# Kernel tuning notes

Measured on AMD Instinct MI355X. Metric: run time of the kernel, lower is better.

The kernel has to match this reference:

```python
import jax, jax.numpy as jnp
import numpy as np

B, S, D = 32, 1024, 256
K, H, L = 64, 4, 4
KH, DV = K // H, D // H  # pooling key size per head, pooling value size
EPS = 1e-5
SCALE = 1.0 / np.sqrt(K).astype(np.float32)  # both encoder and pooling use sqrt(1/key_size)


def _ln(x, gamma=None, beta=None):
    m = jnp.mean(x, axis=-1, keepdims=True)
    v = jnp.mean(jnp.square(x - m), axis=-1, keepdims=True)
    y = (x - m) * jax.lax.rsqrt(v + EPS)
    if gamma is not None:
        y = y * gamma + beta
    return y


def setup_inputs() -> dict:
    key = jax.random.key(0)
    ks = iter(jax.random.split(key, 32))

    def w(shape, fan_in):
        return jax.random.normal(next(ks), shape, jnp.float32) / np.sqrt(fan_in).astype(np.float32)

    inp = {
        "input": jax.random.normal(next(ks), (B, S, D), jnp.float32),
        "lin0_W": w((D, D), D), "lin0_b": jnp.zeros((D,), jnp.float32),
        # stacked params for the 4 AttentionEncoder layers
        "enc_Wk": w((L, D, K), D), "enc_bk": jnp.zeros((L, K), jnp.float32),
        "enc_Wq": w((L, D, K), D), "enc_bq": jnp.zeros((L, K), jnp.float32),
        "enc_Wv": w((L, D, D), D), "enc_bv": jnp.zeros((L, D), jnp.float32),
        "enc_Wb": w((L, D, 1), D), "enc_bb": jnp.zeros((L, 1), jnp.float32),
        "enc_Wff": w((L, D, D), D), "enc_bff": jnp.zeros((L, D), jnp.float32),
        "enc_g1": jnp.ones((L, D), jnp.float32), "enc_beta1": jnp.zeros((L, D), jnp.float32),
        # multi-head pooling head
        "pool_Wk": w((D, KH), D), "pool_bk": jnp.zeros((KH,), jnp.float32),
        "pool_Wv": w((D, DV), D), "pool_bv": jnp.zeros((DV,), jnp.float32),
        "queries": jax.random.normal(next(ks), (H, KH), jnp.float32),
        "lin1_W": w((D, 2), D), "lin1_b": jnp.zeros((2,), jnp.float32),
    }
    return inp


def reference(input, lin0_W, lin0_b, enc_Wk, enc_bk, enc_Wq, enc_bq, enc_Wv, enc_bv,
              enc_Wb, enc_bb, enc_Wff, enc_bff, enc_g1, enc_beta1,
              pool_Wk, pool_bk, pool_Wv, pool_bv, queries, lin1_W, lin1_b):
    # NOTE: original code computes act0(lin0(input)) and then discards it (dead code);
    # it is omitted here since it does not affect the output.
    x = input
    for i in range(L):
        k = (x @ enc_Wk[i] + enc_bk[i]) * SCALE          # [B,S,K]
        q = x @ enc_Wq[i] + enc_bq[i]                     # [B,S,K]
        v = x @ enc_Wv[i] + enc_bv[i]                     # [B,S,D]
        bias = x @ enc_Wb[i] + enc_bb[i]                  # [B,S,1], broadcast over columns
        scores = jax.nn.sigmoid(jnp.einsum('bik,bjk->bij', k, q) + bias)  # [B,S,S]
        attn = jnp.einsum('bij,bjd->bid', scores, v)      # [B,S,D]
        res = _ln(x + attn, enc_g1[i], enc_beta1[i])
        ff = jax.nn.relu(res @ enc_Wff[i] + enc_bff[i])
        x = _ln(res + ff)                                 # norm2: no affine
    # multi-head pooling with learned queries
    pk = (x @ pool_Wk + pool_bk) * SCALE                  # [B,S,KH]
    pv = x @ pool_Wv + pool_bv                            # [B,S,DV]
    sc = jnp.einsum('bsk,hk->bsh', pk, queries)           # [B,S,H]
    sc = jax.nn.softmax(sc, axis=1)                       # softmax over sequence
    pooled = jnp.einsum('bsh,bsd->bhd', sc, pv).reshape(x.shape[0], -1)  # [B, H*DV]=[B,D]
    return pooled @ lin1_W + lin1_b                       # [B,2]
```

## Files before the change

kernel.cpp:

```cpp
#include <hip/hip_runtime.h>
#include <hip/hip_bf16.h>
#include <math.h>

#define BB 32
#define SS 1024
#define DD 256
#define MM (BB*SS)
#define LEPS 1e-5f

typedef __bf16 bf16x8 __attribute__((ext_vector_type(8)));
typedef __bf16 bf16x4 __attribute__((ext_vector_type(4)));
typedef float f32x4 __attribute__((ext_vector_type(4)));

__global__ __launch_bounds__(256) void cast_wt(const float* __restrict__ W,
                                               __bf16* __restrict__ WT,
                                               int N, float scale, int dstride, int noff) {
    int n = blockIdx.x, l = blockIdx.z, k = threadIdx.x;
    WT[(size_t)dstride * l + (size_t)(n + noff) * 256 + k] =
        (__bf16)(W[(size_t)256 * N * l + (size_t)k * N + n] * scale);
}

__global__ __launch_bounds__(128) void bias_combine(const float* __restrict__ bk,
                                                    const float* __restrict__ bq,
                                                    float* __restrict__ dst) {
    int l = blockIdx.x, j = threadIdx.x;
    dst[l * 128 + j] = (j < 64) ? bk[l * 64 + j] * 0.125f : bq[l * 64 + (j - 64)];
}

__global__ __launch_bounds__(256) void cast_x(const float* __restrict__ x, __bf16* __restrict__ xb) {
    size_t i = ((size_t)blockIdx.x * 256 + threadIdx.x) * 8;
    float4 a = *(const float4*)(x + i);
    float4 b = *(const float4*)(x + i + 4);
    __bf16 o[8] __attribute__((aligned(16)));
    o[0] = (__bf16)a.x; o[1] = (__bf16)a.y; o[2] = (__bf16)a.z; o[3] = (__bf16)a.w;
    o[4] = (__bf16)b.x; o[5] = (__bf16)b.y; o[6] = (__bf16)b.z; o[7] = (__bf16)b.w;
    *(bf16x8*)(xb + i) = *(bf16x8*)o;
}

template <int BN, int MODE>
__global__ __launch_bounds__(256) void gemm_mfma(const __bf16* __restrict__ A,
                                                 const __bf16* __restrict__ WT,
                                                 const float* __restrict__ bias,
                                                 float bscale, int relu,
                                                 void* __restrict__ Cv, void* __restrict__ Cv2,
                                                 int N) {
    constexpr int MR = (BN == 128) ? 4 : 2;
    constexpr int NC = (BN == 128) ? 4 : BN / 16;
    const int t = threadIdx.x;
    const int w = t >> 6, lane = t & 63;
    const int m0 = blockIdx.x * 128;
    const int n0 = blockIdx.y * BN;
    const size_t wt_z = (MODE == 3) ? (size_t)blockIdx.z * SS * 256 : 0;
    const size_t c_z  = (MODE == 3) ? (size_t)blockIdx.z * 256 * (size_t)N : 0;
    const int wr = (BN == 128) ? (w >> 1) * 64 : w * 32;
    const int wc = (BN == 128) ? (w & 1) * 64 : 0;
    __shared__ __align__(16) __bf16 Al[128][64];
    __shared__ __align__(16) __bf16 Wl[BN][64];
    f32x4 acc[MR][NC] = {};

    for (int k0 = 0; k0 < 256; k0 += 64) {
        __syncthreads();
        {
            int r = t >> 1, half = t & 1;
            const __bf16* src = A + (size_t)(m0 + r) * 256 + k0 + half * 32;
            bf16x8 v0 = *(const bf16x8*)(src);
            bf16x8 v1 = *(const bf16x8*)(src + 8);
            bf16x8 v2 = *(const bf16x8*)(src + 16);
            bf16x8 v3 = *(const bf16x8*)(src + 24);
            int cb = half * 4;
            *(bf16x8*)&Al[r][((cb + 0) ^ (r & 7)) * 8] = v0;
            *(bf16x8*)&Al[r][((cb + 1) ^ (r & 7)) * 8] = v1;
            *(bf16x8*)&Al[r][((cb + 2) ^ (r & 7)) * 8] = v2;
            *(bf16x8*)&Al[r][((cb + 3) ^ (r & 7)) * 8] = v3;
        }
        if (BN == 128) {
            int r = t >> 1, half = t & 1;
            const __bf16* src = WT + wt_z + (size_t)(n0 + r) * 256 + k0 + half * 32;
            bf16x8 v0 = *(const bf16x8*)(src);
            bf16x8 v1 = *(const bf16x8*)(src + 8);
            bf16x8 v2 = *(const bf16x8*)(src + 16);
            bf16x8 v3 = *(const bf16x8*)(src + 24);
            int cb = half * 4;
            *(bf16x8*)&Wl[r][((cb + 0) ^ (r & 7)) * 8] = v0;
            *(bf16x8*)&Wl[r][((cb + 1) ^ (r & 7)) * 8] = v1;
            *(bf16x8*)&Wl[r][((cb + 2) ^ (r & 7)) * 8] = v2;
            *(bf16x8*)&Wl[r][((cb + 3) ^ (r & 7)) * 8] = v3;
        } else if (BN == 64) {
            int n = t >> 2, q = t & 3;
            const __bf16* src = WT + (size_t)(n0 + n) * 256 + k0 + q * 16;
            bf16x8 v0 = *(const bf16x8*)src;
            bf16x8 v1 = *(const bf16x8*)(src + 8);
            *(bf16x8*)&Wl[n][((q * 2 + 0) ^ (n & 7)) * 8] = v0;
            *(bf16x8*)&Wl[n][((q * 2 + 1) ^ (n & 7)) * 8] = v1;
        } else {
            if (t < 128) {
                int n = t >> 3, c = t & 7;
                bf16x8 v = *(const bf16x8*)(WT + (size_t)(n0 + n) * 256 + k0 + c * 8);
                *(bf16x8*)&Wl[n][(c ^ (n & 7)) * 8] = v;
            }
        }
        __syncthreads();
#pragma unroll
        for (int ks = 0; ks < 2; ks++) {
            int c = ks * 4 + (lane >> 4);
            bf16x8 af[MR];
#pragma unroll
            for (int mf = 0; mf < MR; mf++) {
                int i = wr + mf * 16 + (lane & 15);
                af[mf] = *(const bf16x8*)&Al[i][(c ^ (i & 7)) * 8];
            }
#pragma unroll
            for (int nf = 0; nf < NC; nf++) {
                int n = wc + nf * 16 + (lane & 15);
                bf16x8 bfr = *(const bf16x8*)&Wl[n][(c ^ (n & 7)) * 8];
#pragma unroll
                for (int mf = 0; mf < MR; mf++)
                    acc[mf][nf] = __builtin_amdgcn_mfma_f32_16x16x32_bf16(af[mf], bfr, acc[mf][nf], 0, 0, 0);
            }
        }
    }
#pragma unroll
    for (int mf = 0; mf < MR; mf++) {
#pragma unroll
        for (int nf = 0; nf < NC; nf++) {
            int col = n0 + wc + nf * 16 + (lane & 15);
            float bcol = (MODE == 3) ? 0.f : bias[col] * bscale;
#pragma unroll
            for (int r = 0; r < 4; r++) {
                int row = m0 + wr + mf * 16 + (lane >> 4) * 4 + r;
                float v = acc[mf][nf][r] + ((MODE == 3) ? bias[row] : bcol);
                if (relu) v = fmaxf(v, 0.f);
                if (MODE == 2) {
                    if (col < 64) ((__bf16*)Cv)[(size_t)row * 64 + col] = (__bf16)v;
                    else ((__bf16*)Cv2)[(size_t)row * 64 + (col - 64)] = (__bf16)v;
                } else if (MODE == 1 || MODE == 3) {
                    ((__bf16*)Cv)[c_z + (size_t)row * N + col] = (__bf16)v;
                } else {
                    ((float*)Cv)[(size_t)row * N + col] = v;
                }
            }
        }
    }
}

__global__ __launch_bounds__(256) void bias_gemv(const __bf16* __restrict__ X,
                                                 const float* __restrict__ Wb,
                                                 const float* __restrict__ bb,
                                                 float* __restrict__ out) {
    int wave = threadIdx.x >> 6, lane = threadIdx.x & 63;
    size_t row = (size_t)blockIdx.x * 4 + wave;
    bf16x4 xv = *(const bf16x4*)(X + row * 256 + lane * 4);
    float4 wv = *(const float4*)(Wb + lane * 4);
    float p = (float)xv[0] * wv.x + (float)xv[1] * wv.y + (float)xv[2] * wv.z + (float)xv[3] * wv.w;
    for (int off = 32; off; off >>= 1) p += __shfl_down(p, off, 64);
    if (lane == 0) out[row] = p + bb[0];
}

__global__ __launch_bounds__(512, 4) void attn_mfma(const __bf16* __restrict__ kb,
                                                    const __bf16* __restrict__ qb,
                                                    const __bf16* __restrict__ vT,
                                                    const float* __restrict__ biasb,
                                                    const __bf16* __restrict__ xinb,
                                                    const float* __restrict__ gamma,
                                                    const float* __restrict__ beta,
                                                    __bf16* __restrict__ outb) {
    int h = blockIdx.x;
    int blow = h & 7, rest = h >> 3;
    int ib = rest & 15;
    int b = blow + (rest >> 4) * 8;
    const int i0 = ib * 64;
    const int t = threadIdx.x;
    const int w = t >> 6, lane = t & 63;
    const int iq = w >> 1;
    const int dhalf = w & 1;

    __shared__ __align__(16) __bf16 Kl[64][64];
    __shared__ __align__(16) __bf16 Ql[64][64];
    __shared__ __align__(16) __bf16 Vl[256][64];
    __shared__ __align__(16) __bf16 Sl[64][64];
    __shared__ float bsh[64];
    __shared__ float rowred[2][64][2];

    const int qj = t >> 3, qc = t & 7;
    const __bf16* qsrc_base = qb + ((size_t)(b * SS + qj)) * 64 + qc * 8;
    const int vd = t >> 1, vjh = t & 1;
    const __bf16* vsrc_base = vT + ((size_t)b * 256 + vd) * SS + vjh * 32;

    {
        int i = t >> 3, c = t & 7;
        bf16x8 v = *(const bf16x8*)(kb + ((size_t)(b * SS + i0 + i)) * 64 + c * 8);
        *(bf16x8*)&Kl[i][(c ^ (i & 7)) * 8] = v;
        if (t < 64) bsh[t] = biasb[b * SS + i0 + t];
    }
    {
        bf16x8 qv = *(const bf16x8*)(qsrc_base);
        *(bf16x8*)&Ql[qj][(qc ^ (qj & 7)) * 8] = qv;
#pragma unroll
        for (int u = 0; u < 4; u++) {
            bf16x8 v = *(const bf16x8*)(vsrc_base + u * 8);
            *(bf16x8*)&Vl[vd][((vjh * 4 + u) ^ (vd & 7)) * 8] = v;
        }
    }
    __syncthreads();

    f32x4 acc[8] = {};

    for (int j0 = 0; j0 < SS; j0 += 64) {
        const bool has_next = (j0 + 64) < SS;
        bf16x8 qn;
        bf16x8 vn0, vn1, vn2, vn3;
        if (has_next) {
            qn = *(const bf16x8*)(qsrc_base + (size_t)(j0 + 64) * 64);
            const __bf16* vs = vsrc_base + j0 + 64;
            vn0 = *(const bf16x8*)(vs);
            vn1 = *(const bf16x8*)(vs + 8);
            vn2 = *(const bf16x8*)(vs + 16);
            vn3 = *(const bf16x8*)(vs + 24);
        }
#pragma unroll
        for (int jj = 0; jj < 2; jj++) {
            int jq = (w & 1) * 2 + jj;
            f32x4 sacc = {0.f, 0.f, 0.f, 0.f};
            __builtin_amdgcn_s_setprio(1);
#pragma unroll
            for (int ks = 0; ks < 2; ks++) {
                int i = iq * 16 + (lane & 15);
                int ck = ks * 4 + (lane >> 4);
                bf16x8 a = *(const bf16x8*)&Kl[i][(ck ^ (i & 7)) * 8];
                int j = jq * 16 + (lane & 15);
                bf16x8 bq = *(const bf16x8*)&Ql[j][(ck ^ (j & 7)) * 8];
                sacc = __builtin_amdgcn_mfma_f32_16x16x32_bf16(a, bq, sacc, 0, 0, 0);
            }
            __builtin_amdgcn_s_setprio(0);
            int jcol = jq * 16 + (lane & 15);
#pragma unroll
            for (int r = 0; r < 4; r++) {
                int irow = iq * 16 + (lane >> 4) * 4 + r;
                float x = sacc[r] + bsh[irow];
                float sg = 1.f / (1.f + __expf(-x));
                Sl[irow][(((jcol >> 3) ^ (irow & 7)) * 8) + (jcol & 7)] = (__bf16)sg;
            }
        }
        __syncthreads();
        bf16x8 am[2];
#pragma unroll
        for (int m = 0; m < 2; m++) {
            int i = iq * 16 + (lane & 15);
            int cj = m * 4 + (lane >> 4);
            am[m] = *(const bf16x8*)&Sl[i][(cj ^ (i & 7)) * 8];
        }
        __builtin_amdgcn_s_setprio(1);
#pragma unroll
        for (int dq = 0; dq < 8; dq++) {
            int d = dhalf * 128 + dq * 16 + (lane & 15);
#pragma unroll
            for (int m = 0; m < 2; m++) {
                int cj = m * 4 + (lane >> 4);
                bf16x8 bv = *(const bf16x8*)&Vl[d][(cj ^ (d & 7)) * 8];
                acc[dq] = __builtin_amdgcn_mfma_f32_16x16x32_bf16(am[m], bv, acc[dq], 0, 0, 0);
            }
        }
        __builtin_amdgcn_s_setprio(0);
        __syncthreads();
        if (has_next) {
            *(bf16x8*)&Ql[qj][(qc ^ (qj & 7)) * 8] = qn;
            *(bf16x8*)&Vl[vd][((vjh * 4 + 0) ^ (vd & 7)) * 8] = vn0;
            *(bf16x8*)&Vl[vd][((vjh * 4 + 1) ^ (vd & 7)) * 8] = vn1;
            *(bf16x8*)&Vl[vd][((vjh * 4 + 2) ^ (vd & 7)) * 8] = vn2;
            *(bf16x8*)&Vl[vd][((vjh * 4 + 3) ^ (vd & 7)) * 8] = vn3;
            __syncthreads();
        }
    }

#pragma unroll
    for (int r = 0; r < 4; r++) {
        int il = iq * 16 + (lane >> 4) * 4 + r;
        size_t rowoff = ((size_t)(b * SS + i0 + il)) * 256 + dhalf * 128 + (lane & 15);
#pragma unroll
        for (int dq = 0; dq < 8; dq++)
            acc[dq][r] += (float)xinb[rowoff + dq * 16];
    }
    float sr[4], qr[4];
#pragma unroll
    for (int r = 0; r < 4; r++) {
        float s = 0.f, q = 0.f;
#pragma unroll
        for (int dq = 0; dq < 8; dq++) {
            float v = acc[dq][r];
            s += v; q += v * v;
        }
#pragma unroll
        for (int mask = 8; mask; mask >>= 1) {
            s += __shfl_xor(s, mask, 64);
            q += __shfl_xor(q, mask, 64);
        }
        sr[r] = s; qr[r] = q;
    }
    if ((lane & 15) == 0) {
#pragma unroll
        for (int r = 0; r < 4; r++) {
            int il = iq * 16 + (lane >> 4) * 4 + r;
            rowred[dhalf][il][0] = sr[r];
            rowred[dhalf][il][1] = qr[r];
        }
    }
    __syncthreads();
    float gv[8], bv2[8];
#pragma unroll
    for (int dq = 0; dq < 8; dq++) {
        int d = dhalf * 128 + dq * 16 + (lane & 15);
        gv[dq] = gamma[d];
        bv2[dq] = beta[d];
    }
#pragma unroll
    for (int r = 0; r < 4; r++) {
        int il = iq * 16 + (lane >> 4) * 4 + r;
        float st = rowred[0][il][0] + rowred[1][il][0];
        float qt = rowred[0][il][1] + rowred[1][il][1];
        float mean = st * (1.f / 256.f);
        float var = qt * (1.f / 256.f) - mean * mean;
        float inv = 1.f / sqrtf(var + LEPS);
        size_t rowoff = ((size_t)(b * SS + i0 + il)) * 256 + dhalf * 128 + (lane & 15);
#pragma unroll
        for (int dq = 0; dq < 8; dq++) {
            float o = (acc[dq][r] - mean) * inv * gv[dq] + bv2[dq];
            outb[rowoff + dq * 16] = (__bf16)o;
        }
    }
}

__global__ __launch_bounds__(512) void gemm_ff_ln2(const __bf16* __restrict__ A,
                                                   const __bf16* __restrict__ WT,
                                                   const float* __restrict__ bias,
                                                   const __bf16* __restrict__ resid,
                                                   __bf16* __restrict__ outb) {
    const int t = threadIdx.x;
    const int w = t >> 6, lane = t & 63;
    const int m0 = blockIdx.x * 128;
    const int wr = (w >> 2) * 64, wc = (w & 3) * 64;
    __shared__ __align__(16) __bf16 Al[128][64];
    __shared__ __align__(16) __bf16 Wl[256][64];
    __shared__ float rowred[4][128][2];
    f32x4 acc[4][4] = {};

    for (int k0 = 0; k0 < 256; k0 += 64) {
        __syncthreads();
        {
            int r = t >> 2, c0 = (t & 3) * 2;
            const __bf16* src = A + (size_t)(m0 + r) * 256 + k0 + c0 * 8;
            bf16x8 v0 = *(const bf16x8*)src;
            bf16x8 v1 = *(const bf16x8*)(src + 8);
            *(bf16x8*)&Al[r][((c0 + 0) ^ (r & 7)) * 8] = v0;
            *(bf16x8*)&Al[r][((c0 + 1) ^ (r & 7)) * 8] = v1;
        }
        {
            int n = t >> 1, c0 = (t & 1) * 4;
            const __bf16* src = WT + (size_t)n * 256 + k0 + c0 * 8;
#pragma unroll
            for (int u = 0; u < 4; u++) {
                bf16x8 v = *(const bf16x8*)(src + u * 8);
                *(bf16x8*)&Wl[n][((c0 + u) ^ (n & 7)) * 8] = v;
            }
        }
        __syncthreads();
#pragma unroll
        for (int ks = 0; ks < 2; ks++) {
            int c = ks * 4 + (lane >> 4);
            bf16x8 af[4];
#pragma unroll
            for (int mf = 0; mf < 4; mf++) {
                int i = wr + mf * 16 + (lane & 15);
                af[mf] = *(const bf16x8*)&Al[i][(c ^ (i & 7)) * 8];
            }
#pragma unroll
            for (int nf = 0; nf < 4; nf++) {
                int n = wc + nf * 16 + (lane & 15);
                bf16x8 bfr = *(const bf16x8*)&Wl[n][(c ^ (n & 7)) * 8];
#pragma unroll
                for (int mf = 0; mf < 4; mf++)
                    acc[mf][nf] = __builtin_amdgcn_mfma_f32_16x16x32_bf16(af[mf], bfr, acc[mf][nf], 0, 0, 0);
            }
        }
    }
    float colb[4];
#pragma unroll
    for (int nf = 0; nf < 4; nf++) colb[nf] = bias[wc + nf * 16 + (lane & 15)];
#pragma unroll
    for (int mf = 0; mf < 4; mf++) {
#pragma unroll
        for (int r = 0; r < 4; r++) {
            int rl = wr + mf * 16 + (lane >> 4) * 4 + r;
            const __bf16* rrow = resid + (size_t)(m0 + rl) * 256 + wc + (lane & 15);
            float s = 0.f, q = 0.f;
#pragma unroll
            for (int nf = 0; nf < 4; nf++) {
                float v = fmaxf(acc[mf][nf][r] + colb[nf], 0.f) + (float)rrow[nf * 16];
                acc[mf][nf][r] = v;
                s += v; q += v * v;
            }
#pragma unroll
            for (int msk = 1; msk <= 8; msk <<= 1) {
                s += __shfl_xor(s, msk, 64);
                q += __shfl_xor(q, msk, 64);
            }
            if ((lane & 15) == 0) {
                rowred[w & 3][rl][0] = s;
                rowred[w & 3][rl][1] = q;
            }
        }
    }
    __syncthreads();
#pragma unroll
    for (int mf = 0; mf < 4; mf++) {
#pragma unroll
        for (int r = 0; r < 4; r++) {
            int rl = wr + mf * 16 + (lane >> 4) * 4 + r;
            float s = rowred[0][rl][0] + rowred[1][rl][0] + rowred[2][rl][0] + rowred[3][rl][0];
            float q = rowred[0][rl][1] + rowred[1][rl][1] + rowred[2][rl][1] + rowred[3][rl][1];
            float mean = s * (1.f / 256.f);
            float var = q * (1.f / 256.f) - mean * mean;
            float inv = 1.f / sqrtf(var + LEPS);
            size_t base = (size_t)(m0 + rl) * 256 + wc + (lane & 15);
#pragma unroll
            for (int nf = 0; nf < 4; nf++) {
                float o = (acc[mf][nf][r] - mean) * inv;
                outb[base + nf * 16] = (__bf16)o;
            }
        }
    }
}

__global__ __launch_bounds__(1024) void pool_kernel(const float* __restrict__ pk,
                                                    const float* __restrict__ pv,
                                                    const float* __restrict__ queries,
                                                    const float* __restrict__ W1,
                                                    const float* __restrict__ b1,
                                                    float* __restrict__ out) {
    const int b = blockIdx.x;
    const int t = threadIdx.x;
    __shared__ float sc[4][1024];
    __shared__ float qv[4][16];
    __shared__ float redsum[4];
    __shared__ float psum[4][256];
    __shared__ float r0[256], r1[256];
    if (t < 64) qv[t >> 4][t & 15] = queries[t];
    __syncthreads();
    {
        int s = t;
        const float* p = pk + ((size_t)b * SS + s) * 16;
        float4 a0 = *(const float4*)p;
        float4 a1 = *(const float4*)(p + 4);
        float4 a2 = *(const float4*)(p + 8);
        float4 a3 = *(const float4*)(p + 12);
#pragma unroll
        for (int hh = 0; hh < 4; hh++) {
            float d = a0.x * qv[hh][0] + a0.y * qv[hh][1] + a0.z * qv[hh][2] + a0.w * qv[hh][3]
                    + a1.x * qv[hh][4] + a1.y * qv[hh][5] + a1.z * qv[hh][6] + a1.w * qv[hh][7]
                    + a2.x * qv[hh][8] + a2.y * qv[hh][9] + a2.z * qv[hh][10] + a2.w * qv[hh][11]
                    + a3.x * qv[hh][12] + a3.y * qv[hh][13] + a3.z * qv[hh][14] + a3.w * qv[hh][15];
            sc[hh][s] = d;
        }
    }
    __syncthreads();
    if (t < 256) {
        int hh = t >> 6, lane = t & 63;
        float m = -1e30f;
        for (int s = lane; s < 1024; s += 64) m = fmaxf(m, sc[hh][s]);
        for (int off = 32; off; off >>= 1) m = fmaxf(m, __shfl_down(m, off, 64));
        m = __shfl(m, 0, 64);
        float sum = 0.f;
        for (int s = lane; s < 1024; s += 64) {
            float e = expf(sc[hh][s] - m);
            sc[hh][s] = e;
            sum += e;
        }
        for (int off = 32; off; off >>= 1) sum += __shfl_down(sum, off, 64);
        if (lane == 0) redsum[hh] = sum;
    }
    __syncthreads();
    {
        int chunk = t >> 8, pair = t & 255;
        int hh = pair >> 6, d = pair & 63;
        float a = 0.f;
        int s0 = chunk * 256;
        for (int s = s0; s < s0 + 256; s++)
            a += sc[hh][s] * pv[((size_t)b * SS + s) * 64 + d];
        psum[chunk][pair] = a;
    }
    __syncthreads();
    if (t < 256) {
        float a = (psum[0][t] + psum[1][t] + psum[2][t] + psum[3][t]) / redsum[t >> 6];
        r0[t] = a * W1[t * 2 + 0];
        r1[t] = a * W1[t * 2 + 1];
    }
    __syncthreads();
    for (int off = 128; off > 0; off >>= 1) {
        if (t < off) { r0[t] += r0[t + off]; r1[t] += r1[t + off]; }
        __syncthreads();
    }
    if (t == 0) {
        out[b * 2 + 0] = r0[0] + b1[0];
        out[b * 2 + 1] = r1[0] + b1[1];
    }
}

extern "C" void kernel_launch(void* const* d_in, const int* in_sizes, int n_in,
                              void* d_out, int out_size, void* d_ws, size_t ws_size,
                              hipStream_t stream) {
    const float* input = (const float*)d_in[0];
    const float* eWk = (const float*)d_in[3];
    const float* ebk = (const float*)d_in[4];
    const float* eWq = (const float*)d_in[5];
    const float* ebq = (const float*)d_in[6];
    const float* eWv = (const float*)d_in[7];
    const float* ebv = (const float*)d_in[8];
    const float* eWb = (const float*)d_in[9];
    const float* ebb = (const float*)d_in[10];
    const float* eWff = (const float*)d_in[11];
    const float* ebff = (const float*)d_in[12];
    const float* eg1 = (const float*)d_in[13];
    const float* ebe1 = (const float*)d_in[14];
    const float* pWk = (const float*)d_in[15];
    const float* pbk = (const float*)d_in[16];
    const float* pWv = (const float*)d_in[17];
    const float* pbv = (const float*)d_in[18];
    const float* qrs = (const float*)d_in[19];
    const float* W1 = (const float*)d_in[20];
    const float* b1 = (const float*)d_in[21];
    float* out = (float*)d_out;

    float* ws = (float*)d_ws;
    float* xbuf = ws;
    __bf16* xbf = (__bf16*)(xbuf + (size_t)MM * DD);
    float* tmp2 = (float*)(xbf + (size_t)MM * DD);
    float* r3 = tmp2 + (size_t)MM * DD;
    __bf16* tmp2bf = (__bf16*)r3;
    __bf16* vTb = tmp2bf + (size_t)MM * DD;
    float* r4 = r3 + (size_t)MM * DD;
    __bf16* kbf = (__bf16*)r4;
    __bf16* qbf = kbf + (size_t)MM * 64;
    float* bbuf = r4 + (size_t)MM * (DD / 2);
    __bf16* wbf = (__bf16*)(bbuf + MM);

    __bf16* WkqT = wbf;
    __bf16* WvT = WkqT + 4 * 128 * 256;
    __bf16* WffT = WvT + 4 * 256 * 256;
    __bf16* pWkT = WffT + 4 * 256 * 256;
    __bf16* pWvT = pWkT + 16 * 256;
    float* biasc = (float*)(pWvT + 64 * 256);

    float* pkbuf = tmp2;
    float* pvbuf = tmp2 + (size_t)MM * 16;

    const float SC = 0.125f;

    cast_wt<<<dim3(64, 1, 4), 256, 0, stream>>>(eWk, WkqT, 64, SC, 128 * 256, 0);
    cast_wt<<<dim3(64, 1, 4), 256, 0, stream>>>(eWq, WkqT, 64, 1.f, 128 * 256, 64);
    cast_wt<<<dim3(256, 1, 4), 256, 0, stream>>>(eWv, WvT, 256, 1.f, 256 * 256, 0);
    cast_wt<<<dim3(256, 1, 4), 256, 0, stream>>>(eWff, WffT, 256, 1.f, 256 * 256, 0);
    cast_wt<<<dim3(16, 1, 1), 256, 0, stream>>>(pWk, pWkT, 16, SC, 16 * 256, 0);
    cast_wt<<<dim3(64, 1, 1), 256, 0, stream>>>(pWv, pWvT, 64, 1.f, 64 * 256, 0);
    bias_combine<<<4, 128, 0, stream>>>(ebk, ebq, biasc);
    cast_x<<<MM * DD / (256 * 8), 256, 0, stream>>>(input, xbf);

    for (int l = 0; l < 4; l++) {
        gemm_mfma<128, 2><<<dim3(MM / 128, 1), 256, 0, stream>>>(
            xbf, WkqT + (size_t)l * 128 * 256, biasc + l * 128, 1.f, 0, kbf, qbf, 64);
        gemm_mfma<128, 3><<<dim3(2, SS / 128, BB), 256, 0, stream>>>(
            WvT + (size_t)l * 256 * 256, xbf, ebv + l * DD, 1.f, 0, vTb, nullptr, SS);
        bias_gemv<<<MM / 4, 256, 0, stream>>>(xbf, eWb + (size_t)l * DD, ebb + l, bbuf);
        attn_mfma<<<dim3(512, 1), 512, 0, stream>>>(kbf, qbf, vTb, bbuf, xbf,
                                                    eg1 + l * DD, ebe1 + l * DD, tmp2bf);
        gemm_ff_ln2<<<dim3(MM / 128, 1), 512, 0, stream>>>(
            tmp2bf, WffT + (size_t)l * 256 * 256, ebff + l * DD, tmp2bf, xbf);
    }
    gemm_mfma<16, 0><<<dim3(MM / 128, 1), 256, 0, stream>>>(xbf, pWkT, pbk, SC, 0, pkbuf, nullptr, 16);
    gemm_mfma<64, 0><<<dim3(MM / 128, 1), 256, 0, stream>>>(xbf, pWvT, pbv, 1.f, 0, pvbuf, nullptr, 64);
    pool_kernel<<<BB, 1024, 0, stream>>>(pkbuf, pvbuf, qrs, W1, b1, out);
}
```

Before: 488.0 us.

## Re-split attention PV tiles across warps and parallelize pooling into three kernels

In the attention kernel, each of the 8 warps now owns a 32-column slice of D across all 64 query rows, instead of a 16-row by 128-column tile. Each V fragment loaded from LDS is therefore reused across 4 row groups, and the LayerNorm reduction is rebuilt to combine partial sums from all 8 warps. The pooling head, which was a single 32-block kernel, is split into a softmax kernel, a chunked weighted-sum kernel, and a final reduction kernel. The split gives the GPU more blocks to run at once, at the cost of extra launches and intermediate buffers in global memory.

Measured after the change: 477.8 us. 1.02x faster.

```diff
diff --git a/kernel.cpp b/kernel.cpp
--- a/kernel.cpp
+++ b/kernel.cpp
@@ -172,14 +172,13 @@
     const int t = threadIdx.x;
     const int w = t >> 6, lane = t & 63;
     const int iq = w >> 1;
-    const int dhalf = w & 1;
 
     __shared__ __align__(16) __bf16 Kl[64][64];
     __shared__ __align__(16) __bf16 Ql[64][64];
     __shared__ __align__(16) __bf16 Vl[256][64];
     __shared__ __align__(16) __bf16 Sl[64][64];
     __shared__ float bsh[64];
-    __shared__ float rowred[2][64][2];
+    __shared__ float rowred[8][64][2];
 
     const int qj = t >> 3, qc = t & 7;
     const __bf16* qsrc_base = qb + ((size_t)(b * SS + qj)) * 64 + qc * 8;
@@ -203,7 +202,7 @@
     }
     __syncthreads();
 
-    f32x4 acc[8] = {};
+    f32x4 acc[4][2] = {};
 
     for (int j0 = 0; j0 < SS; j0 += 64) {
         const bool has_next = (j0 + 64) < SS;
@@ -242,22 +241,23 @@
             }
         }
         __syncthreads();
-        bf16x8 am[2];
+        __builtin_amdgcn_s_setprio(1);
 #pragma unroll
         for (int m = 0; m < 2; m++) {
-            int i = iq * 16 + (lane & 15);
             int cj = m * 4 + (lane >> 4);
-            am[m] = *(const bf16x8*)&Sl[i][(cj ^ (i & 7)) * 8];
-        }
-        __builtin_amdgcn_s_setprio(1);
-#pragma unroll
-        for (int dq = 0; dq < 8; dq++) {
-            int d = dhalf * 128 + dq * 16 + (lane & 15);
-#pragma unroll
-            for (int m = 0; m < 2; m++) {
-                int cj = m * 4 + (lane >> 4);
+            bf16x8 am[4];
+#pragma unroll
+            for (int ig = 0; ig < 4; ig++) {
+                int i = ig * 16 + (lane & 15);
+                am[ig] = *(const bf16x8*)&Sl[i][(cj ^ (i & 7)) * 8];
+            }
+#pragma unroll
+            for (int dt = 0; dt < 2; dt++) {
+                int d = w * 32 + dt * 16 + (lane & 15);
                 bf16x8 bv = *(const bf16x8*)&Vl[d][(cj ^ (d & 7)) * 8];
-                acc[dq] = __builtin_amdgcn_mfma_f32_16x16x32_bf16(am[m], bv, acc[dq], 0, 0, 0);
+#pragma unroll
+                for (int ig = 0; ig < 4; ig++)
+                    acc[ig][dt] = __builtin_amdgcn_mfma_f32_16x16x32_bf16(am[ig], bv, acc[ig][dt], 0, 0, 0);
             }
         }
         __builtin_amdgcn_s_setprio(0);
@@ -273,58 +273,45 @@
     }
 
 #pragma unroll
-    for (int r = 0; r < 4; r++) {
-        int il = iq * 16 + (lane >> 4) * 4 + r;
-        size_t rowoff = ((size_t)(b * SS + i0 + il)) * 256 + dhalf * 128 + (lane & 15);
-#pragma unroll
-        for (int dq = 0; dq < 8; dq++)
-            acc[dq][r] += (float)xinb[rowoff + dq * 16];
-    }
-    float sr[4], qr[4];
-#pragma unroll
-    for (int r = 0; r < 4; r++) {
-        float s = 0.f, q = 0.f;
-#pragma unroll
-        for (int dq = 0; dq < 8; dq++) {
-            float v = acc[dq][r];
-            s += v; q += v * v;
-        }
-#pragma unroll
-        for (int mask = 8; mask; mask >>= 1) {
-            s += __shfl_xor(s, mask, 64);
-            q += __shfl_xor(q, mask, 64);
-        }
-        sr[r] = s; qr[r] = q;
-    }
-    if ((lane & 15) == 0) {
+    for (int ig = 0; ig < 4; ig++) {
 #pragma unroll
         for (int r = 0; r < 4; r++) {
-            int il = iq * 16 + (lane >> 4) * 4 + r;
-            rowred[dhalf][il][0] = sr[r];
-            rowred[dhalf][il][1] = qr[r];
-        }
-    }
-    __syncthreads();
-    float gv[8], bv2[8];
-#pragma unroll
-    for (int dq = 0; dq < 8; dq++) {
-        int d = dhalf * 128 + dq * 16 + (lane & 15);
-        gv[dq] = gamma[d];
-        bv2[dq] = beta[d];
-    }
-#pragma unroll
-    for (int r = 0; r < 4; r++) {
-        int il = iq * 16 + (lane >> 4) * 4 + r;
-        float st = rowred[0][il][0] + rowred[1][il][0];
-        float qt = rowred[0][il][1] + rowred[1][il][1];
-        float mean = st * (1.f / 256.f);
-        float var = qt * (1.f / 256.f) - mean * mean;
-        float inv = 1.f / sqrtf(var + LEPS);
-        size_t rowoff = ((size_t)(b * SS + i0 + il)) * 256 + dhalf * 128 + (lane & 15);
-#pragma unroll
-        for (int dq = 0; dq < 8; dq++) {
-            float o = (acc[dq][r] - mean) * inv * gv[dq] + bv2[dq];
-            outb[rowoff + dq * 16] = (__bf16)o;
+            int il = ig * 16 + (lane >> 4) * 4 + r;
+            size_t rowoff = ((size_t)(b * SS + i0 + il)) * 256 + w * 32 + (lane & 15);
+            float v0 = acc[ig][0][r] + (float)xinb[rowoff];
+            float v1 = acc[ig][1][r] + (float)xinb[rowoff + 16];
+            acc[ig][0][r] = v0; acc[ig][1][r] = v1;
+            float s = v0 + v1, q = v0 * v0 + v1 * v1;
+#pragma unroll
+            for (int mask = 8; mask; mask >>= 1) {
+                s += __shfl_xor(s, mask, 64);
+                q += __shfl_xor(q, mask, 64);
+            }
+            if ((lane & 15) == 0) {
+                rowred[w][il][0] = s;
+                rowred[w][il][1] = q;
+            }
+        }
+    }
+    __syncthreads();
+    float gv0 = gamma[w * 32 + (lane & 15)];
+    float gv1 = gamma[w * 32 + 16 + (lane & 15)];
+    float be0 = beta[w * 32 + (lane & 15)];
+    float be1 = beta[w * 32 + 16 + (lane & 15)];
+#pragma unroll
+    for (int ig = 0; ig < 4; ig++) {
+#pragma unroll
+        for (int r = 0; r < 4; r++) {
+            int il = ig * 16 + (lane >> 4) * 4 + r;
+            float s = 0.f, q = 0.f;
+#pragma unroll
+            for (int ww = 0; ww < 8; ww++) { s += rowred[ww][il][0]; q += rowred[ww][il][1]; }
+            float mean = s * (1.f / 256.f);
+            float var = q * (1.f / 256.f) - mean * mean;
+            float inv = 1.f / sqrtf(var + LEPS);
+            size_t rowoff = ((size_t)(b * SS + i0 + il)) * 256 + w * 32 + (lane & 15);
+            outb[rowoff]      = (__bf16)((acc[ig][0][r] - mean) * inv * gv0 + be0);
+            outb[rowoff + 16] = (__bf16)((acc[ig][1][r] - mean) * inv * gv1 + be1);
         }
     }
 }
@@ -430,69 +417,72 @@
     }
 }
 
-__global__ __launch_bounds__(1024) void pool_kernel(const float* __restrict__ pk,
-                                                    const float* __restrict__ pv,
+__global__ __launch_bounds__(256) void pool_softmax(const float* __restrict__ pk,
                                                     const float* __restrict__ queries,
-                                                    const float* __restrict__ W1,
-                                                    const float* __restrict__ b1,
-                                                    float* __restrict__ out) {
-    const int b = blockIdx.x;
+                                                    float* __restrict__ wout) {
+    const int b = blockIdx.x, h = blockIdx.y;
     const int t = threadIdx.x;
-    __shared__ float sc[4][1024];
-    __shared__ float qv[4][16];
-    __shared__ float redsum[4];
-    __shared__ float psum[4][256];
-    __shared__ float r0[256], r1[256];
-    if (t < 64) qv[t >> 4][t & 15] = queries[t];
-    __syncthreads();
-    {
-        int s = t;
+    const int wv = t >> 6, lane = t & 63;
+    __shared__ float qv[16];
+    __shared__ float redm[4], reds[4];
+    if (t < 16) qv[t] = queries[h * 16 + t];
+    __syncthreads();
+    float sc[4];
+#pragma unroll
+    for (int c = 0; c < 4; c++) {
+        int s = c * 256 + t;
         const float* p = pk + ((size_t)b * SS + s) * 16;
         float4 a0 = *(const float4*)p;
         float4 a1 = *(const float4*)(p + 4);
         float4 a2 = *(const float4*)(p + 8);
         float4 a3 = *(const float4*)(p + 12);
-#pragma unroll
-        for (int hh = 0; hh < 4; hh++) {
-            float d = a0.x * qv[hh][0] + a0.y * qv[hh][1] + a0.z * qv[hh][2] + a0.w * qv[hh][3]
-                    + a1.x * qv[hh][4] + a1.y * qv[hh][5] + a1.z * qv[hh][6] + a1.w * qv[hh][7]
-                    + a2.x * qv[hh][8] + a2.y * qv[hh][9] + a2.z * qv[hh][10] + a2.w * qv[hh][11]
-                    + a3.x * qv[hh][12] + a3.y * qv[hh][13] + a3.z * qv[hh][14] + a3.w * qv[hh][15];
-            sc[hh][s] = d;
-        }
-    }
-    __syncthreads();
-    if (t < 256) {
-        int hh = t >> 6, lane = t & 63;
-        float m = -1e30f;
-        for (int s = lane; s < 1024; s += 64) m = fmaxf(m, sc[hh][s]);
-        for (int off = 32; off; off >>= 1) m = fmaxf(m, __shfl_down(m, off, 64));
-        m = __shfl(m, 0, 64);
-        float sum = 0.f;
-        for (int s = lane; s < 1024; s += 64) {
-            float e = expf(sc[hh][s] - m);
-            sc[hh][s] = e;
-            sum += e;
-        }
-        for (int off = 32; off; off >>= 1) sum += __shfl_down(sum, off, 64);
-        if (lane == 0) redsum[hh] = sum;
-    }
-    __syncthreads();
-    {
-        int chunk = t >> 8, pair = t & 255;
-        int hh = pair >> 6, d = pair & 63;
-        float a = 0.f;
-        int s0 = chunk * 256;
-        for (int s = s0; s < s0 + 256; s++)
-            a += sc[hh][s] * pv[((size_t)b * SS + s) * 64 + d];
-        psum[chunk][pair] = a;
-    }
-    __syncthreads();
-    if (t < 256) {
-        float a = (psum[0][t] + psum[1][t] + psum[2][t] + psum[3][t]) / redsum[t >> 6];
-        r0[t] = a * W1[t * 2 + 0];
-        r1[t] = a * W1[t * 2 + 1];
-    }
+        sc[c] = a0.x * qv[0] + a0.y * qv[1] + a0.z * qv[2] + a0.w * qv[3]
+              + a1.x * qv[4] + a1.y * qv[5] + a1.z * qv[6] + a1.w * qv[7]
+              + a2.x * qv[8] + a2.y * qv[9] + a2.z * qv[10] + a2.w * qv[11]
+              + a3.x * qv[12] + a3.y * qv[13] + a3.z * qv[14] + a3.w * qv[15];
+    }
+    float m = fmaxf(fmaxf(sc[0], sc[1]), fmaxf(sc[2], sc[3]));
+    for (int off = 32; off; off >>= 1) m = fmaxf(m, __shfl_xor(m, off, 64));
+    if (lane == 0) redm[wv] = m;
+    __syncthreads();
+    m = fmaxf(fmaxf(redm[0], redm[1]), fmaxf(redm[2], redm[3]));
+    float e[4];
+    float sum = 0.f;
+#pragma unroll
+    for (int c = 0; c < 4; c++) { e[c] = expf(sc[c] - m); sum += e[c]; }
+    for (int off = 32; off; off >>= 1) sum += __shfl_xor(sum, off, 64);
+    if (lane == 0) reds[wv] = sum;
+    __syncthreads();
+    float inv = 1.f / (reds[0] + reds[1] + reds[2] + reds[3]);
+#pragma unroll
+    for (int c = 0; c < 4; c++)
+        wout[((size_t)(b * 4 + h)) * SS + c * 256 + t] = e[c] * inv;
+}
+
+__global__ __launch_bounds__(256) void pool_wsum(const float* __restrict__ wgt,
+                                                 const float* __restrict__ pv,
+                                                 float* __restrict__ partial) {
+    const int b = blockIdx.x, c = blockIdx.y;
+    const int h = threadIdx.x >> 6, d = threadIdx.x & 63;
+    const float* wrow = wgt + ((size_t)(b * 4 + h)) * SS + c * 64;
+    const float* pvb = pv + ((size_t)(b * SS + c * 64)) * 64 + d;
+    float a = 0.f;
+#pragma unroll 8
+    for (int s = 0; s < 64; s++) a += wrow[s] * pvb[(size_t)s * 64];
+    partial[((size_t)b * 16 + c) * 256 + threadIdx.x] = a;
+}
+
+__global__ __launch_bounds__(256) void pool_final(const float* __restrict__ partial,
+                                                  const float* __restrict__ W1,
+                                                  const float* __restrict__ b1,
+                                                  float* __restrict__ out) {
+    const int b = blockIdx.x, t = threadIdx.x;
+    __shared__ float r0[256], r1[256];
+    float a = 0.f;
+#pragma unroll
+    for (int c = 0; c < 16; c++) a += partial[((size_t)b * 16 + c) * 256 + t];
+    r0[t] = a * W1[t * 2 + 0];
+    r1[t] = a * W1[t * 2 + 1];
     __syncthreads();
     for (int off = 128; off > 0; off >>= 1) {
         if (t < off) { r0[t] += r0[t + off]; r1[t] += r1[t + off]; }
@@ -551,6 +541,8 @@
 
     float* pkbuf = tmp2;
     float* pvbuf = tmp2 + (size_t)MM * 16;
+    float* wgtbuf = tmp2 + (size_t)MM * 80;
+    float* partial = wgtbuf + (size_t)BB * 4 * SS;
 
     const float SC = 0.125f;
 
@@ -576,5 +568,7 @@
     }
     gemm_mfma<16, 0><<<dim3(MM / 128, 1), 256, 0, stream>>>(xbf, pWkT, pbk, SC, 0, pkbuf, nullptr, 16);
     gemm_mfma<64, 0><<<dim3(MM / 128, 1), 256, 0, stream>>>(xbf, pWvT, pbv, 1.f, 0, pvbuf, nullptr, 64);
-    pool_kernel<<<BB, 1024, 0, stream>>>(pkbuf, pvbuf, qrs, W1, b1, out);
-}
+    pool_softmax<<<dim3(BB, 4), 256, 0, stream>>>(pkbuf, qrs, wgtbuf);
+    pool_wsum<<<dim3(BB, 16), 256, 0, stream>>>(wgtbuf, pvbuf, partial);
+    pool_final<<<BB, 256, 0, stream>>>(partial, W1, b1, out);
+}
```
